# Kernel optimization log

Measured on AMD Instinct MI355X. Metric: run time of the kernel, lower is better.

## Reference

```python
import jax, jax.numpy as jnp
import numpy as np

DIM = 1024
HEADS = 16
EPS = 1e-5


def layer_norm(x, gamma, beta):
    mu = jnp.mean(x, axis=-1, keepdims=True)
    var = jnp.mean(jnp.square(x - mu), axis=-1, keepdims=True)
    return (x - mu) * jax.lax.rsqrt(var + EPS) * gamma + beta


def setup_inputs() -> dict:
    key = jax.random.key(0)
    ks = jax.random.split(key, 9)
    B, Nq, Nk = 8, 1024, 1024
    s = 1.0 / np.sqrt(DIM)
    return {
        "x": jax.random.normal(ks[0], (B, Nq, DIM), jnp.float32),
        "context": jax.random.normal(ks[1], (B, Nk, DIM), jnp.float32),
        "relative_position_bias": jax.random.normal(ks[2], (HEADS, Nq, Nk), jnp.float32),
        "Wq": jax.random.normal(ks[3], (DIM, DIM), jnp.float32) * s,
        "Wk": jax.random.normal(ks[4], (DIM, DIM), jnp.float32) * s,
        "Wv": jax.random.normal(ks[5], (DIM, DIM), jnp.float32) * s,
        "Wo": jax.random.normal(ks[6], (DIM, DIM), jnp.float32) * s,
        "bo": jnp.zeros((DIM,), jnp.float32),
        "gamma": jnp.ones((DIM,), jnp.float32),
        "beta": jnp.zeros((DIM,), jnp.float32),
    }


def reference(x, context, relative_position_bias, Wq, Wk, Wv, Wo, bo, gamma, beta):
    h = HEADS
    d = DIM // h
    scale = d ** -0.5
    xn = layer_norm(x, gamma, beta)
    cn = layer_norm(context, gamma, beta)
    B, Nq, _ = x.shape
    Nk = context.shape[1]
    # b n (h d) -> b h n d
    q = (xn @ Wq).reshape(B, Nq, h, d).transpose(0, 2, 1, 3)
    k = (cn @ Wk).reshape(B, Nk, h, d).transpose(0, 2, 1, 3)
    v = (cn @ Wv).reshape(B, Nk, h, d).transpose(0, 2, 1, 3)
    scores = jnp.einsum('bhid,bhjd->bhij', q, k) * scale
    scores = scores + relative_position_bias[None]
    attn = jax.nn.softmax(scores, axis=-1)
    out = jnp.einsum('bhij,bhjd->bhid', attn, v)
    out = out.transpose(0, 2, 1, 3).reshape(B, Nq, h * d)
    return out @ Wo + bo
```

## Files before the change

### kernel.cpp

```cpp
#include <hip/hip_runtime.h>
#include <hip/hip_bf16.h>
#include <stdint.h>

#define DIM   1024
#define HEADS 16
#define HD    64
#define NB    8
#define NTOK  1024
#define MROWS (NB*NTOK)

#define LOG2E 1.4426950408889634f
#define SCL   (0.125f * LOG2E)

typedef __attribute__((ext_vector_type(8))) _Float16 f16x8;
typedef __attribute__((ext_vector_type(4))) _Float16 f16x4;
typedef __attribute__((ext_vector_type(4))) float    f32x4;

typedef unsigned int uint_as1 __attribute__((address_space(1)));
typedef unsigned int uint_as3 __attribute__((address_space(3)));

__device__ __forceinline__ void gload16(const void* g, void* l) {
    __builtin_amdgcn_global_load_lds((const uint_as1*)g, (uint_as3*)l, 16, 0, 0);
}

__device__ __forceinline__ unsigned pkrtz(float a, float b) {
    auto h = __builtin_amdgcn_cvt_pkrtz(a, b);
    return __builtin_bit_cast(unsigned, h);
}

#if __has_builtin(__builtin_amdgcn_permlane32_swap)
__device__ __forceinline__ void swap32(unsigned& a, unsigned& b) {
    auto r = __builtin_amdgcn_permlane32_swap(a, b, false, false);
    a = r[0]; b = r[1];
}
#else
__device__ __forceinline__ void swap32(unsigned& a, unsigned& b) {
    unsigned as = (unsigned)__shfl_xor((int)a, 32, 64);
    unsigned bs = (unsigned)__shfl_xor((int)b, 32, 64);
    bool lo = ((threadIdx.x & 63) < 32);
    unsigned na = lo ? a : bs, nb = lo ? as : b;
    a = na; b = nb;
}
#endif
#if __has_builtin(__builtin_amdgcn_permlane16_swap)
__device__ __forceinline__ void swap16(unsigned& a, unsigned& b) {
    auto r = __builtin_amdgcn_permlane16_swap(a, b, false, false);
    a = r[0]; b = r[1];
}
#else
__device__ __forceinline__ void swap16(unsigned& a, unsigned& b) {
    unsigned as = (unsigned)__shfl_xor((int)a, 16, 64);
    unsigned bs = (unsigned)__shfl_xor((int)b, 16, 64);
    bool ev = ((threadIdx.x & 16) == 0);
    unsigned na = ev ? a : bs, nb = ev ? as : b;
    a = na; b = nb;
}
#endif
__device__ __forceinline__ float redsum32(float x) {
    unsigned a = __builtin_bit_cast(unsigned, x), b = a;
    swap32(a, b);
    return __builtin_bit_cast(float, a) + __builtin_bit_cast(float, b);
}
__device__ __forceinline__ float redsum16(float x) {
    unsigned a = __builtin_bit_cast(unsigned, x), b = a;
    swap16(a, b);
    return __builtin_bit_cast(float, a) + __builtin_bit_cast(float, b);
}

__global__ __launch_bounds__(256) void prep_kernel(const float* __restrict__ x,
                                                   const float* __restrict__ ctx,
                                                   const float* __restrict__ gamma,
                                                   const float* __restrict__ beta,
                                                   _Float16* __restrict__ xn,
                                                   _Float16* __restrict__ cn,
                                                   const float* __restrict__ Wq, const float* __restrict__ Wk,
                                                   const float* __restrict__ Wv, const float* __restrict__ Wo,
                                                   _Float16* __restrict__ Tq, _Float16* __restrict__ Tk,
                                                   _Float16* __restrict__ Tv, _Float16* __restrict__ To) {
    __shared__ float redm[8];
    __shared__ float tile[32][33];
    int bid = blockIdx.x;
    int t = threadIdx.x;
    if (bid < 2 * MROWS) {
        int row = bid;
        const float* src; _Float16* dst;
        if (row < MROWS) { src = x + (size_t)row * DIM;   dst = xn + (size_t)row * DIM; }
        else             { int r = row - MROWS;
                           src = ctx + (size_t)r * DIM;   dst = cn + (size_t)r * DIM; }
        float4 v = *(const float4*)(src + t * 4);
        float s  = v.x + v.y + v.z + v.w;
        float s2 = v.x*v.x + v.y*v.y + v.z*v.z + v.w*v.w;
        #pragma unroll
        for (int o = 32; o; o >>= 1) { s += __shfl_xor(s, o, 64); s2 += __shfl_xor(s2, o, 64); }
        int w = t >> 6, l = t & 63;
        if (l == 0) { redm[w] = s; redm[4 + w] = s2; }
        __syncthreads();
        s  = redm[0] + redm[1] + redm[2] + redm[3];
        s2 = redm[4] + redm[5] + redm[6] + redm[7];
        float mu   = s * (1.0f / DIM);
        float rstd = rsqrtf(s2 * (1.0f / DIM) - mu * mu + 1e-5f);
        float4 g  = *(const float4*)(gamma + t * 4);
        float4 bb = *(const float4*)(beta  + t * 4);
        f16x4 o;
        o[0] = (_Float16)((v.x - mu) * rstd * g.x + bb.x);
        o[1] = (_Float16)((v.y - mu) * rstd * g.y + bb.y);
        o[2] = (_Float16)((v.z - mu) * rstd * g.z + bb.z);
        o[3] = (_Float16)((v.w - mu) * rstd * g.w + bb.w);
        *(f16x4*)(dst + t * 4) = o;
    } else {
        int fid = bid - 2 * MROWS;
        int m = fid >> 10;
        int rem = fid & 1023;
        int j0 = (rem & 31) * 32, k0 = (rem >> 5) * 32;
        const float* W = (m == 0) ? Wq : (m == 1) ? Wk : (m == 2) ? Wv : Wo;
        _Float16*    T = (m == 0) ? Tq : (m == 1) ? Tk : (m == 2) ? Tv : To;
        int tx = t & 31, ty = t >> 5;
        #pragma unroll
        for (int i = 0; i < 4; i++) tile[ty + i*8][tx] = W[(size_t)(k0 + ty + i*8) * DIM + j0 + tx];
        __syncthreads();
        #pragma unroll
        for (int i = 0; i < 4; i++) T[(size_t)(j0 + ty + i*8) * DIM + k0 + tx] = (_Float16)tile[tx][ty + i*8];
    }
}

__global__ __launch_bounds__(256) void gemm_qkv(const _Float16* __restrict__ xn,
                                                const _Float16* __restrict__ cn,
                                                const _Float16* __restrict__ wqT,
                                                const _Float16* __restrict__ wkT,
                                                const _Float16* __restrict__ wvT,
                                                _Float16* __restrict__ qbf,
                                                _Float16* __restrict__ kbf,
                                                _Float16* __restrict__ vtb) {
    __shared__ _Float16 As[128 * 64];
    __shared__ _Float16 Bs[128 * 64];
    const int K = DIM;
    int mode = blockIdx.y >> 3;
    int n0 = (blockIdx.y & 7) * 128;
    int m0 = blockIdx.x * 128;
    const _Float16* A  = (mode == 0) ? xn : cn;
    const _Float16* BT = (mode == 0) ? wqT : (mode == 1) ? wkT : wvT;
    int t = threadIdx.x, w = t >> 6, l = t & 63;
    int wr = w >> 1, wc = w & 1, ln = l & 15, qtr = l >> 4;
    f32x4 acc[4][4] = {};
    int srow = w * 8 + (l >> 3);
    int cg   = (l & 7) ^ (srow & 7);
    const _Float16* Ag = A  + (size_t)(m0 + srow) * K + cg * 8;
    const _Float16* Bg = BT + (size_t)(n0 + srow) * K + cg * 8;
    for (int kt = 0; kt < K; kt += 64) {
        #pragma unroll
        for (int p = 0; p < 4; p++) {
            gload16(Ag + (size_t)(p * 32) * K, &As[(p * 32 + w * 8) * 64]);
            gload16(Bg + (size_t)(p * 32) * K, &Bs[(p * 32 + w * 8) * 64]);
        }
        Ag += 64; Bg += 64;
        __syncthreads();
        #pragma unroll
        for (int kk = 0; kk < 2; kk++) {
            f16x8 af[4], bfr[4];
            #pragma unroll
            for (int r = 0; r < 4; r++)
                af[r]  = *(const f16x8*)&As[(wr * 64 + r * 16 + ln) * 64 + (((qtr + kk*4) ^ (ln & 7)) * 8)];
            #pragma unroll
            for (int c = 0; c < 4; c++)
                bfr[c] = *(const f16x8*)&Bs[(wc * 64 + c * 16 + ln) * 64 + (((qtr + kk*4) ^ (ln & 7)) * 8)];
            #pragma unroll
            for (int r = 0; r < 4; r++)
                #pragma unroll
                for (int c = 0; c < 4; c++)
                    acc[r][c] = __builtin_amdgcn_mfma_f32_16x16x32_f16(af[r], bfr[c], acc[r][c], 0, 0, 0);
        }
        __syncthreads();
    }
    #pragma unroll
    for (int r = 0; r < 4; r++)
        #pragma unroll
        for (int c = 0; c < 4; c++) {
            int gn = n0 + wc * 64 + c * 16 + ln;
            int h = gn >> 6, d = gn & 63;
            #pragma unroll
            for (int q = 0; q < 4; q++) {
                int gm = m0 + wr * 64 + r * 16 + qtr * 4 + q;
                int b = gm >> 10, n = gm & 1023;
                float v = acc[r][c][q];
                if (mode == 0)
                    qbf[(((size_t)(b * HEADS + h) * NTOK + n) << 6) + d] = (_Float16)(v * SCL);
                else if (mode == 1)
                    kbf[(((size_t)(b * HEADS + h) * NTOK + n) << 6) + d] = (_Float16)v;
                else
                    vtb[(((size_t)(b * HEADS + h) * HD + d) << 10) + n] = (_Float16)v;
            }
        }
}

__global__ __launch_bounds__(256) void gemm_out(const _Float16* __restrict__ A,
                                                const _Float16* __restrict__ BT,
                                                float* __restrict__ Cout,
                                                const float* __restrict__ bias) {
    __shared__ _Float16 As[128 * 64];
    __shared__ _Float16 Bs[128 * 64];
    const int K = DIM;
    int m0 = blockIdx.x * 128, n0 = blockIdx.y * 128;
    int t = threadIdx.x, w = t >> 6, l = t & 63;
    int wr = w >> 1, wc = w & 1, ln = l & 15, qtr = l >> 4;
    f32x4 acc[4][4] = {};
    int srow = w * 8 + (l >> 3);
    int cg   = (l & 7) ^ (srow & 7);
    const _Float16* Ag = A  + (size_t)(m0 + srow) * K + cg * 8;
    const _Float16* Bg = BT + (size_t)(n0 + srow) * K + cg * 8;
    for (int kt = 0; kt < K; kt += 64) {
        #pragma unroll
        for (int p = 0; p < 4; p++) {
            gload16(Ag + (size_t)(p * 32) * K, &As[(p * 32 + w * 8) * 64]);
            gload16(Bg + (size_t)(p * 32) * K, &Bs[(p * 32 + w * 8) * 64]);
        }
        Ag += 64; Bg += 64;
        __syncthreads();
        #pragma unroll
        for (int kk = 0; kk < 2; kk++) {
            f16x8 af[4], bfr[4];
            #pragma unroll
            for (int r = 0; r < 4; r++)
                af[r]  = *(const f16x8*)&As[(wr * 64 + r * 16 + ln) * 64 + (((qtr + kk*4) ^ (ln & 7)) * 8)];
            #pragma unroll
            for (int c = 0; c < 4; c++)
                bfr[c] = *(const f16x8*)&Bs[(wc * 64 + c * 16 + ln) * 64 + (((qtr + kk*4) ^ (ln & 7)) * 8)];
            #pragma unroll
            for (int r = 0; r < 4; r++)
                #pragma unroll
                for (int c = 0; c < 4; c++)
                    acc[r][c] = __builtin_amdgcn_mfma_f32_16x16x32_f16(af[r], bfr[c], acc[r][c], 0, 0, 0);
        }
        __syncthreads();
    }
    #pragma unroll
    for (int r = 0; r < 4; r++)
        #pragma unroll
        for (int c = 0; c < 4; c++) {
            int gn = n0 + wc * 64 + c * 16 + ln;
            float bv = bias[gn];
            #pragma unroll
            for (int q = 0; q < 4; q++) {
                int gm = m0 + wr * 64 + r * 16 + qtr * 4 + q;
                Cout[(size_t)gm * DIM + gn] = acc[r][c][q] + bv;
            }
        }
}

__global__ __launch_bounds__(256) void attn_kernel(const _Float16* __restrict__ qb,
                                                   const _Float16* __restrict__ kb,
                                                   const _Float16* __restrict__ vt,
                                                   const float* __restrict__ bias,
                                                   _Float16* __restrict__ ao) {
    __shared__ _Float16 Kt[2][64 * 64];
    __shared__ _Float16 Vs[2][64 * 64];
    int bid = blockIdx.x;
    int rem = bid >> 3;
    int h = (bid & 7) * 2 + (rem & 1);
    int b = (rem >> 1) & 7;
    int qt = rem >> 4;
    int q0 = qt * 64;
    int t = threadIdx.x, w = t >> 6, l = t & 63, ln = l & 15, qtr = l >> 4;
    const _Float16* qbase = qb + (size_t)(b * HEADS + h) * NTOK * HD;
    const _Float16* kbase = kb + (size_t)(b * HEADS + h) * NTOK * HD;
    const _Float16* vbase = vt + (size_t)(b * HEADS + h) * HD * NTOK;
    const float*    bbase = bias + ((size_t)h * NTOK + q0 + w * 16) * NTOK;

    f16x8 qfr[2];
    #pragma unroll
    for (int ks = 0; ks < 2; ks++)
        qfr[ks] = *(const f16x8*)&qbase[(size_t)(q0 + w*16 + ln) * HD + ks*32 + qtr*8];

#define STAGE(BUF, J0) do {                                                     \
        int rb_ = w * 16;                                                       \
        _Float16* kl_ = &Kt[BUF][rb_ * 64];                                     \
        _Float16* vl_ = &Vs[BUF][rb_ * 64];                                     \
        int r_ = rb_ + (l >> 3); int cg_ = (l & 7) ^ (r_ & 7);                  \
        gload16(kbase + (size_t)((J0) + r_) * HD + cg_ * 8, kl_);               \
        gload16(vbase + (size_t)r_ * NTOK + (J0) + cg_ * 8, vl_);               \
        r_ += 8; cg_ = (l & 7) ^ (r_ & 7);                                      \
        gload16(kbase + (size_t)((J0) + r_) * HD + cg_ * 8, kl_ + 8 * 64);      \
        gload16(vbase + (size_t)r_ * NTOK + (J0) + cg_ * 8, vl_ + 8 * 64);      \
    } while (0)

#define LOADB(DST, TT) do {                                                     \
        _Pragma("unroll")                                                       \
        for (int r_ = 0; r_ < 4; r_++)                                          \
            DST[r_] = *(const float4*)&bbase[(size_t)ln * NTOK                  \
                                             + (TT)*64 + qtr*4 + r_*16];        \
    } while (0)

    STAGE(0, 0);
    float4 bpp[2][4];
    LOADB(bpp[0], 0);
    __syncthreads();

    float l_part = 0.f;
    f32x4 acc[4] = {};

    #pragma unroll 2
    for (int tt = 0; tt < 16; tt++) {
        int cur = tt & 1;
        if (tt < 15) { STAGE(cur ^ 1, (tt + 1) * 64); LOADB(bpp[cur ^ 1], tt + 1); }

        f32x4 st2[4];
        #pragma unroll
        for (int r = 0; r < 4; r++) {
            float4 bb = bpp[cur][r];
            f32x4 ci = {bb.x * LOG2E, bb.y * LOG2E, bb.z * LOG2E, bb.w * LOG2E};
            st2[r] = ci;
        }
        __builtin_amdgcn_s_setprio(1);
        #pragma unroll
        for (int r = 0; r < 4; r++) {
            int row = r * 16 + ln;
            #pragma unroll
            for (int ks = 0; ks < 2; ks++) {
                f16x8 kf = *(const f16x8*)&Kt[cur][row * 64 + (((qtr + ks*4) ^ (ln & 7)) * 8)];
                st2[r] = __builtin_amdgcn_mfma_f32_16x16x32_f16(kf, qfr[ks], st2[r], 0, 0, 0);
            }
        }
        __builtin_amdgcn_s_setprio(0);

        float sig = 0.f;
        unsigned pk2[4][2];
        #pragma unroll
        for (int r = 0; r < 4; r++) {
            float p0 = exp2f(st2[r][0]);
            float p1 = exp2f(st2[r][1]);
            float p2 = exp2f(st2[r][2]);
            float p3 = exp2f(st2[r][3]);
            sig += (p0 + p1) + (p2 + p3);
            pk2[r][0] = pkrtz(p0, p1);
            pk2[r][1] = pkrtz(p2, p3);
        }
        l_part += sig;

        f16x8 pfr[2];
        #pragma unroll
        for (int ks = 0; ks < 2; ks++) {
            unsigned pw[4];
            #pragma unroll
            for (int c = 0; c < 2; c++) {
                unsigned U = pk2[2*ks][c], T = pk2[2*ks + 1][c];
                swap32(U, T);
                swap16(U, T);
                pw[c]     = U;
                pw[2 + c] = T;
            }
            pfr[ks] = __builtin_bit_cast(f16x8, *(const uint4*)pw);
        }

        __builtin_amdgcn_s_setprio(1);
        #pragma unroll
        for (int dg = 0; dg < 4; dg++) {
            int row = dg * 16 + ln;
            #pragma unroll
            for (int ks = 0; ks < 2; ks++) {
                f16x8 vf = *(const f16x8*)&Vs[cur][row * 64 + (((qtr + ks*4) ^ (ln & 7)) * 8)];
                acc[dg] = __builtin_amdgcn_mfma_f32_16x16x32_f16(pfr[ks], vf, acc[dg], 0, 0, 0);
            }
        }
        __builtin_amdgcn_s_setprio(0);
        __syncthreads();
    }

    float inv = 1.0f / redsum16(redsum32(l_part));
    float invm[4];
    #pragma unroll
    for (int m = 0; m < 4; m++) invm[m] = __shfl(inv, (l & 48) | (qtr * 4 + m), 64);
    size_t rowb = (size_t)b * NTOK + q0 + w * 16 + qtr * 4;
    #pragma unroll
    for (int dg = 0; dg < 4; dg++)
        #pragma unroll
        for (int m = 0; m < 4; m++)
            ao[(rowb + m) * DIM + h * HD + dg * 16 + ln] = (_Float16)(acc[dg][m] * invm[m]);
#undef STAGE
#undef LOADB
}

extern "C" void kernel_launch(void* const* d_in, const int* in_sizes, int n_in,
                              void* d_out, int out_size, void* d_ws, size_t ws_size,
                              hipStream_t stream) {
    const float* x     = (const float*)d_in[0];
    const float* ctx   = (const float*)d_in[1];
    const float* bias  = (const float*)d_in[2];
    const float* Wq    = (const float*)d_in[3];
    const float* Wk    = (const float*)d_in[4];
    const float* Wv    = (const float*)d_in[5];
    const float* Wo    = (const float*)d_in[6];
    const float* bo    = (const float*)d_in[7];
    const float* gamma = (const float*)d_in[8];
    const float* beta  = (const float*)d_in[9];
    float* out = (float*)d_out;

    _Float16* ws  = (_Float16*)d_ws;
    _Float16* xn  = ws;
    _Float16* cn  = xn  + (size_t)MROWS * DIM;
    _Float16* wqT = cn  + (size_t)MROWS * DIM;
    _Float16* wkT = wqT + (size_t)DIM * DIM;
    _Float16* wvT = wkT + (size_t)DIM * DIM;
    _Float16* woT = wvT + (size_t)DIM * DIM;
    _Float16* qbf = woT + (size_t)DIM * DIM;
    _Float16* kbf = qbf + (size_t)MROWS * DIM;
    _Float16* vtb = kbf + (size_t)MROWS * DIM;
    _Float16* aob = vtb + (size_t)MROWS * DIM;

    prep_kernel<<<dim3(2 * MROWS + 4096), dim3(256), 0, stream>>>(
        x, ctx, gamma, beta, xn, cn, Wq, Wk, Wv, Wo, wqT, wkT, wvT, woT);
    gemm_qkv<<<dim3(64, 24), dim3(256), 0, stream>>>(xn, cn, wqT, wkT, wvT, qbf, kbf, vtb);
    attn_kernel<<<dim3(NB * HEADS * 16), dim3(256), 0, stream>>>(qbf, kbf, vtb, bias, aob);
    gemm_out<<<dim3(64, 8), dim3(256), 0, stream>>>(aob, woT, out, bo);
}
```

Baseline: 227.3 us.

## Convert relative position bias to pre-scaled fp16 inside the QKV GEMM launch

The fp32 relative position bias is converted once per call into an fp16 copy pre-multiplied by log2(e). Extra blocks appended to the QKV GEMM grid do this conversion so it overlaps with the GEMM. If the workspace is too small, a separate conversion kernel runs instead. The attention kernel then reads half as many bias bytes across the eight batch passes and skips the per-element scaling multiply. The cost is bias precision reduced to fp16 and an additional write and read of a 32 MB buffer.

```diff
diff --git a/kernel.cpp b/kernel.cpp
--- a/kernel.cpp
+++ b/kernel.cpp
@@ -123,6 +123,19 @@
     }
 }
 
+__global__ __launch_bounds__(256) void biasconv_kernel(const float* __restrict__ bias,
+                                                       _Float16* __restrict__ bias2) {
+    size_t i = ((size_t)blockIdx.x * 256 + threadIdx.x) * 8;
+    float4 a = *(const float4*)(bias + i);
+    float4 b = *(const float4*)(bias + i + 4);
+    f16x8 o;
+    o[0] = (_Float16)(a.x * LOG2E); o[1] = (_Float16)(a.y * LOG2E);
+    o[2] = (_Float16)(a.z * LOG2E); o[3] = (_Float16)(a.w * LOG2E);
+    o[4] = (_Float16)(b.x * LOG2E); o[5] = (_Float16)(b.y * LOG2E);
+    o[6] = (_Float16)(b.z * LOG2E); o[7] = (_Float16)(b.w * LOG2E);
+    *(f16x8*)(bias2 + i) = o;
+}
+
 __global__ __launch_bounds__(256) void gemm_qkv(const _Float16* __restrict__ xn,
                                                 const _Float16* __restrict__ cn,
                                                 const _Float16* __restrict__ wqT,
@@ -130,16 +143,36 @@
                                                 const _Float16* __restrict__ wvT,
                                                 _Float16* __restrict__ qbf,
                                                 _Float16* __restrict__ kbf,
-                                                _Float16* __restrict__ vtb) {
+                                                _Float16* __restrict__ vtb,
+                                                const float* __restrict__ bias,
+                                                _Float16* __restrict__ bias2) {
     __shared__ _Float16 As[128 * 64];
     __shared__ _Float16 Bs[128 * 64];
+    int t = threadIdx.x;
+    if (blockIdx.y >= 24) {
+        int bid = (blockIdx.y - 24) * 64 + blockIdx.x;
+        size_t base = (size_t)bid * 65536 + t * 8;
+        #pragma unroll 4
+        for (int k = 0; k < 32; k++) {
+            size_t i = base + (size_t)k * 2048;
+            float4 a = *(const float4*)(bias + i);
+            float4 b = *(const float4*)(bias + i + 4);
+            f16x8 o;
+            o[0] = (_Float16)(a.x * LOG2E); o[1] = (_Float16)(a.y * LOG2E);
+            o[2] = (_Float16)(a.z * LOG2E); o[3] = (_Float16)(a.w * LOG2E);
+            o[4] = (_Float16)(b.x * LOG2E); o[5] = (_Float16)(b.y * LOG2E);
+            o[6] = (_Float16)(b.z * LOG2E); o[7] = (_Float16)(b.w * LOG2E);
+            *(f16x8*)(bias2 + i) = o;
+        }
+        return;
+    }
     const int K = DIM;
     int mode = blockIdx.y >> 3;
     int n0 = (blockIdx.y & 7) * 128;
     int m0 = blockIdx.x * 128;
     const _Float16* A  = (mode == 0) ? xn : cn;
     const _Float16* BT = (mode == 0) ? wqT : (mode == 1) ? wkT : wvT;
-    int t = threadIdx.x, w = t >> 6, l = t & 63;
+    int w = t >> 6, l = t & 63;
     int wr = w >> 1, wc = w & 1, ln = l & 15, qtr = l >> 4;
     f32x4 acc[4][4] = {};
     int srow = w * 8 + (l >> 3);
@@ -249,7 +282,7 @@
 __global__ __launch_bounds__(256) void attn_kernel(const _Float16* __restrict__ qb,
                                                    const _Float16* __restrict__ kb,
                                                    const _Float16* __restrict__ vt,
-                                                   const float* __restrict__ bias,
+                                                   const _Float16* __restrict__ bias2,
                                                    _Float16* __restrict__ ao) {
     __shared__ _Float16 Kt[2][64 * 64];
     __shared__ _Float16 Vs[2][64 * 64];
@@ -263,7 +296,7 @@
     const _Float16* qbase = qb + (size_t)(b * HEADS + h) * NTOK * HD;
     const _Float16* kbase = kb + (size_t)(b * HEADS + h) * NTOK * HD;
     const _Float16* vbase = vt + (size_t)(b * HEADS + h) * HD * NTOK;
-    const float*    bbase = bias + ((size_t)h * NTOK + q0 + w * 16) * NTOK;
+    const _Float16* bbase = bias2 + ((size_t)h * NTOK + q0 + w * 16) * NTOK;
 
     f16x8 qfr[2];
     #pragma unroll
@@ -285,12 +318,12 @@
 #define LOADB(DST, TT) do {                                                     \
         _Pragma("unroll")                                                       \
         for (int r_ = 0; r_ < 4; r_++)                                          \
-            DST[r_] = *(const float4*)&bbase[(size_t)ln * NTOK                  \
-                                             + (TT)*64 + qtr*4 + r_*16];        \
+            DST[r_] = *(const f16x4*)&bbase[(size_t)ln * NTOK                   \
+                                            + (TT)*64 + qtr*4 + r_*16];         \
     } while (0)
 
     STAGE(0, 0);
-    float4 bpp[2][4];
+    f16x4 bpp[2][4];
     LOADB(bpp[0], 0);
     __syncthreads();
 
@@ -305,8 +338,8 @@
         f32x4 st2[4];
         #pragma unroll
         for (int r = 0; r < 4; r++) {
-            float4 bb = bpp[cur][r];
-            f32x4 ci = {bb.x * LOG2E, bb.y * LOG2E, bb.z * LOG2E, bb.w * LOG2E};
+            f16x4 bb = bpp[cur][r];
+            f32x4 ci = {(float)bb[0], (float)bb[1], (float)bb[2], (float)bb[3]};
             st2[r] = ci;
         }
         __builtin_amdgcn_s_setprio(1);
@@ -404,10 +437,19 @@
     _Float16* kbf = qbf + (size_t)MROWS * DIM;
     _Float16* vtb = kbf + (size_t)MROWS * DIM;
     _Float16* aob = vtb + (size_t)MROWS * DIM;
+    _Float16* wsEnd = aob + (size_t)MROWS * DIM;
+
+    const size_t biasElems = (size_t)HEADS * NTOK * NTOK;
+    const size_t needBytes = ((size_t)(wsEnd - ws) + biasElems) * sizeof(_Float16);
+    bool fused = ws_size >= needBytes;
+    _Float16* bias2 = fused ? wsEnd : ws;
 
     prep_kernel<<<dim3(2 * MROWS + 4096), dim3(256), 0, stream>>>(
         x, ctx, gamma, beta, xn, cn, Wq, Wk, Wv, Wo, wqT, wkT, wvT, woT);
-    gemm_qkv<<<dim3(64, 24), dim3(256), 0, stream>>>(xn, cn, wqT, wkT, wvT, qbf, kbf, vtb);
-    attn_kernel<<<dim3(NB * HEADS * 16), dim3(256), 0, stream>>>(qbf, kbf, vtb, bias, aob);
+    gemm_qkv<<<dim3(64, fused ? 28 : 24), dim3(256), 0, stream>>>(
+        xn, cn, wqT, wkT, wvT, qbf, kbf, vtb, bias, bias2);
+    if (!fused)
+        biasconv_kernel<<<dim3(8192), dim3(256), 0, stream>>>(bias, bias2);
+    attn_kernel<<<dim3(NB * HEADS * 16), dim3(256), 0, stream>>>(qbf, kbf, vtb, bias2, aob);
     gemm_out<<<dim3(64, 8), dim3(256), 0, stream>>>(aob, woT, out, bo);
 }
```

After: 239.6 us. 5.4% more time.
